# Performance work log

Measured on AMD Instinct MI355X. Metric: run time of the kernel, lower is better.

The kernel has to match this reference:

```python
import jax, jax.numpy as jnp
import numpy as np

EPS = 1e-6
R = 8


def _gram_schmidt(U, eps=EPS):
    # Modified Gram-Schmidt over the r columns of U (dim, r), matching the
    # sequential projection loop in HouseholderReflection.get_orthogonal_matrix.
    cols = []
    u0 = U[:, 0]
    cols.append(u0 / (jnp.linalg.norm(u0) + eps))
    r = U.shape[1]
    for i in range(1, r):
        ui = U[:, i]
        for j in range(i):
            ui = ui - jnp.dot(cols[j], ui) * cols[j]
        cols.append(ui / (jnp.linalg.norm(ui) + eps))
    return cols  # list of r unit vectors (dim,)


def _orthogonal_matrix(hra_u, eps=EPS):
    # Q = prod_i (I - 2 u_i u_i^T), applied as rank-1 updates: Q <- Q - 2 (Q u) u^T
    dim = hra_u.shape[0]
    cols = _gram_schmidt(hra_u, eps)
    Q = jnp.eye(dim, dtype=hra_u.dtype)
    for u in cols:
        Q = Q - 2.0 * jnp.outer(Q @ u, u)
    return Q  # (dim, dim)


def setup_inputs() -> dict:
    key = jax.random.key(0)
    k1, k2, k3, k4, k5 = jax.random.split(key, 5)
    N, D_IN, D_HID, D_OUT = 4096, 2048, 8192, 2048
    x = jax.random.normal(k1, (N, D_IN), dtype=jnp.float32)
    hra_u = jax.random.normal(k2, (D_IN, R), dtype=jnp.float32)
    W_random = jax.random.normal(k3, (D_IN, D_HID), dtype=jnp.float32) / np.sqrt(D_IN)
    W_out = jax.random.normal(k4, (D_HID, D_OUT), dtype=jnp.float32) / np.sqrt(D_HID)
    bias = jax.random.normal(k5, (D_OUT,), dtype=jnp.float32)
    return {"x": x, "hra_u": hra_u, "W_random": W_random, "W_out": W_out, "bias": bias}


def reference(x, hra_u, W_random, W_out, bias):
    # y = gelu(x @ (Q @ W_random)) @ W_out + bias  (torch nn.GELU = exact erf gelu)
    Q = _orthogonal_matrix(hra_u)
    W_t = Q @ W_random                      # (D_IN, D_HID)
    h = jax.nn.gelu(x @ W_t, approximate=False)  # (N, D_HID)
    return h @ W_out + bias                 # (N, D_OUT)
```

## Files before the change

### kernel.cpp

```cpp
#include <hip/hip_runtime.h>
#include <hip/hip_bf16.h>

typedef __bf16 bf16;
typedef __bf16 bf16x4 __attribute__((ext_vector_type(4)));
typedef __bf16 bf16x8 __attribute__((ext_vector_type(8)));
typedef float  f32x4  __attribute__((ext_vector_type(4)));

#define GAS __attribute__((address_space(1)))
#define LAS __attribute__((address_space(3)))

#define NROWS 4096
#define DIN   2048
#define DHID  8192
#define DOUT  2048

__device__ __forceinline__ void gload16(const void* g, void* l) {
    __builtin_amdgcn_global_load_lds((GAS void*)g, (LAS void*)l, 16, 0, 0);
}
template <int N> __device__ __forceinline__ void vmw() {
    asm volatile("s_waitcnt vmcnt(%0)" :: "n"(N) : "memory");
}
__device__ __forceinline__ void bsync() {
    asm volatile("" ::: "memory");
    __builtin_amdgcn_s_barrier();
    asm volatile("" ::: "memory");
}

__global__ __launch_bounds__(64) void gs_kernel(const float* __restrict__ U,
                                                float* __restrict__ Vt) {
    __shared__ float Vs[8][DIN];
    const int l = threadIdx.x;
    float u[32];
    for (int r = 0; r < 8; ++r) {
        #pragma unroll
        for (int s = 0; s < 32; ++s) u[s] = U[(size_t)(l * 32 + s) * 8 + r];
        for (int j = 0; j < r; ++j) {
            float d = 0.f;
            #pragma unroll
            for (int s = 0; s < 32; ++s) d += Vs[j][l * 32 + s] * u[s];
            #pragma unroll
            for (int o = 32; o >= 1; o >>= 1) d += __shfl_xor(d, o);
            #pragma unroll
            for (int s = 0; s < 32; ++s) u[s] -= d * Vs[j][l * 32 + s];
        }
        float nr = 0.f;
        #pragma unroll
        for (int s = 0; s < 32; ++s) nr += u[s] * u[s];
        #pragma unroll
        for (int o = 32; o >= 1; o >>= 1) nr += __shfl_xor(nr, o);
        const float inv = 1.f / (sqrtf(nr) + 1e-6f);
        #pragma unroll
        for (int s = 0; s < 32; ++s) {
            float v = u[s] * inv;
            Vs[r][l * 32 + s] = v;
            Vt[r * DIN + l * 32 + s] = v;
        }
        __syncthreads();
    }
}

__global__ __launch_bounds__(256) void p_kernel(const float* __restrict__ W,
                                                const float* __restrict__ Vt,
                                                float* __restrict__ P) {
    const int t = threadIdx.x;
    const int c = blockIdx.x * 64 + (t & 63);
    const int part = t >> 6;
    float acc[8] = {};
    const int i0 = part * 512;
    #pragma unroll 4
    for (int i = i0; i < i0 + 512; ++i) {
        float w = W[(size_t)i * DHID + c];
        #pragma unroll
        for (int r = 0; r < 8; ++r) acc[r] = fmaf(Vt[r * DIN + i], w, acc[r]);
    }
    __shared__ float red[4][8][64];
    #pragma unroll
    for (int r = 0; r < 8; ++r) red[part][r][t & 63] = acc[r];
    __syncthreads();
    for (int idx = t; idx < 512; idx += 256) {
        int r = idx >> 6, cc = idx & 63;
        P[(size_t)r * DHID + blockIdx.x * 64 + cc] =
            red[0][r][cc] + red[1][r][cc] + red[2][r][cc] + red[3][r][cc];
    }
}

__global__ __launch_bounds__(256) void xv_kernel(const float* __restrict__ x,
                                                 const float* __restrict__ Vt,
                                                 float* __restrict__ xV,
                                                 bf16* __restrict__ xb) {
    const int row = blockIdx.x * 4 + (threadIdx.x >> 6);
    const int l = threadIdx.x & 63;
    const float* xr = x + (size_t)row * DIN;
    bf16* xbr = xb + (size_t)row * DIN;
    float acc[8] = {};
    #pragma unroll
    for (int s = 0; s < 8; ++s) {
        const int c0 = (s * 64 + l) * 4;
        float4 v = *(const float4*)&xr[c0];
        bf16x4 o = { (bf16)v.x, (bf16)v.y, (bf16)v.z, (bf16)v.w };
        *(bf16x4*)&xbr[c0] = o;
        #pragma unroll
        for (int r = 0; r < 8; ++r) {
            float4 vt = *(const float4*)&Vt[r * DIN + c0];
            acc[r] = fmaf(v.x, vt.x, fmaf(v.y, vt.y, fmaf(v.z, vt.z, fmaf(v.w, vt.w, acc[r]))));
        }
    }
    #pragma unroll
    for (int r = 0; r < 8; ++r) {
        float d = acc[r];
        #pragma unroll
        for (int o = 32; o >= 1; o >>= 1) d += __shfl_xor(d, o);
        if (l == 0) xV[(size_t)row * 8 + r] = d;
    }
}

__global__ __launch_bounds__(256) void tconv_kernel(const float* __restrict__ in,
                                                    bf16* __restrict__ out,
                                                    int R, int C) {
    __shared__ bf16 tile[64][66];
    const int t = threadIdx.x;
    const int n0 = blockIdx.x * 64, k0 = blockIdx.y * 64;
    const int rr = t >> 4, c4 = (t & 15) * 4;
    #pragma unroll
    for (int q = 0; q < 4; ++q) {
        int row = k0 + rr + q * 16;
        float4 v = *(const float4*)&in[(size_t)row * C + n0 + c4];
        tile[c4 + 0][rr + q * 16] = (bf16)v.x;
        tile[c4 + 1][rr + q * 16] = (bf16)v.y;
        tile[c4 + 2][rr + q * 16] = (bf16)v.z;
        tile[c4 + 3][rr + q * 16] = (bf16)v.w;
    }
    __syncthreads();
    const int n = t >> 2, kk = (t & 3) * 16;
    unsigned int w[8];
    #pragma unroll
    for (int i = 0; i < 8; ++i) w[i] = *(const unsigned int*)&tile[n][kk + i * 2];
    uint4 lo = { w[0], w[1], w[2], w[3] }, hi = { w[4], w[5], w[6], w[7] };
    uint4* dst = (uint4*)&out[(size_t)(n0 + n) * R + k0 + kk];
    dst[0] = lo;
    dst[1] = hi;
}

__global__ __launch_bounds__(256) void redk(float* __restrict__ out,
                                            const float* __restrict__ p1,
                                            const float* __restrict__ bias) {
    const size_t i = (size_t)blockIdx.x * 256 + threadIdx.x;
    float4 a = ((const float4*)out)[i];
    float4 b = ((const float4*)p1)[i];
    const int c4 = (int)(i & (DOUT / 4 - 1)) * 4;
    float4 bb = *(const float4*)&bias[c4];
    float4 r = { a.x + b.x + bb.x, a.y + b.y + bb.y,
                 a.z + b.z + bb.z, a.w + b.w + bb.w };
    ((float4*)out)[i] = r;
}

template <int BM, int BN, int WM, int WN, int CR, int CC, int EPI>
__global__ __launch_bounds__(512) void gemm8p(const bf16* __restrict__ A,
                                              const bf16* __restrict__ Bt,
                                              const int N, const int nk, const int lda,
                                              const float* __restrict__ e0,
                                              const float* __restrict__ e1,
                                              void* __restrict__ Cout) {
    constexpr int MF = BM / (WM * 16);
    constexpr int NF = BN / (WN * 16);
    constexpr int ABYTES = BM * 64;
    constexpr int BUFB = (BM + BN) * 64;
    constexpr int LA = BM / 128, LB = BN / 128, LPT = LA + LB;
    __shared__ __align__(128) char lds[4 * BUFB];

    const int t = threadIdx.x;
    const int wid = t >> 6, lane = t & 63;
    const int wr = wid / WN, wc = wid % WN;
    const int lrow = lane & 15;
    const int lk2 = (lane >> 4) * 16;

    int bid = blockIdx.x, sk = 0;
    if constexpr (EPI == 2) { sk = bid & 1; bid >>= 1; }
    const int chunks_c = (N / BN) / CC;
    const int xc = bid & 7;
    const int ii = bid >> 3;
    const int bm = (xc / chunks_c) * CR + ii / CC;
    const int bn = (xc % chunks_c) * CC + ii % CC;

    const size_t koff = (size_t)sk * nk * 32;
    const bf16* Abase = A + (size_t)bm * BM * lda + koff;
    const bf16* Bbase = Bt + (size_t)bn * BN * lda + koff;

    const int ar0 = wr * (MF * 16) + lrow;
    const unsigned aoff = (unsigned)(ar0 * 64 + lk2) ^ (unsigned)(((ar0 >> 1) & 3) << 4);
    const int br0 = wc * (NF * 16) + lrow;
    const unsigned boff = (unsigned)ABYTES +
        ((unsigned)(br0 * 64 + lk2) ^ (unsigned)(((br0 >> 1) & 3) << 4));

    f32x4 acc[MF][NF] = {};

    auto STAGE = [&](int kt, int part) {
        const size_t ko = (size_t)kt * 32;
        char* dstb = lds + (kt & 3) * BUFB;
        if (part == 0) {
            #pragma unroll
            for (int i2 = 0; i2 < LA; ++i2) {
                const int lin = i2 * 512 + t;
                const int row = lin >> 2;
                const int c16 = (lin & 3) ^ ((lin >> 3) & 3);
                gload16(Abase + (size_t)row * lda + ko + c16 * 8,
                        dstb + (i2 * 512 + (t & 448)) * 16);
            }
        } else {
            #pragma unroll
            for (int i2 = 0; i2 < LB; ++i2) {
                const int lin = i2 * 512 + t;
                const int row = lin >> 2;
                const int c16 = (lin & 3) ^ ((lin >> 3) & 3);
                gload16(Bbase + (size_t)row * lda + ko + c16 * 8,
                        dstb + ABYTES + (i2 * 512 + (t & 448)) * 16);
            }
        }
    };

    auto TILE = [&](int kt, bool dostage) {
        const char* bp = lds + (kt & 3) * BUFB;
        bf16x8 av0[MF / 2], av1[MF / 2], bv[NF];
        #pragma unroll
        for (int m = 0; m < MF / 2; ++m)
            av0[m] = *(const bf16x8*)(bp + aoff + m * 1024);
        #pragma unroll
        for (int n = 0; n < NF; ++n)
            bv[n] = *(const bf16x8*)(bp + boff + n * 1024);
        if (dostage) STAGE(kt + 3, 0);
        __builtin_amdgcn_sched_barrier(0);
        bsync();
        __builtin_amdgcn_s_setprio(1);
        #pragma unroll
        for (int m = 0; m < MF / 2; ++m)
            #pragma unroll
            for (int n = 0; n < NF; ++n)
                acc[m][n] = __builtin_amdgcn_mfma_f32_16x16x32_bf16(av0[m], bv[n], acc[m][n], 0, 0, 0);
        __builtin_amdgcn_s_setprio(0);
        bsync();
        #pragma unroll
        for (int m = 0; m < MF / 2; ++m)
            av1[m] = *(const bf16x8*)(bp + aoff + (m + MF / 2) * 1024);
        if (dostage) STAGE(kt + 3, 1);
        __builtin_amdgcn_sched_barrier(0);
        bsync();
        __builtin_amdgcn_s_setprio(1);
        #pragma unroll
        for (int m = 0; m < MF / 2; ++m)
            #pragma unroll
            for (int n = 0; n < NF; ++n)
                acc[m + MF / 2][n] = __builtin_amdgcn_mfma_f32_16x16x32_bf16(av1[m], bv[n], acc[m + MF / 2][n], 0, 0, 0);
        __builtin_amdgcn_s_setprio(0);
    };

    #pragma unroll
    for (int p = 0; p < 3; ++p) { STAGE(p, 0); STAGE(p, 1); }
    vmw<2 * LPT>(); bsync();
    int kt = 0;
    for (; kt < nk - 3; ++kt) {
        TILE(kt, true);
        vmw<2 * LPT>();
        bsync();
    }
    TILE(kt, false); vmw<LPT>(); bsync(); ++kt;
    TILE(kt, false); vmw<0>();   bsync(); ++kt;
    TILE(kt, false); bsync();

    const int jrow = (lane >> 4) << 2;
    if constexpr (EPI == 1) {
        float* xVl = (float*)lds;
        float* Pl  = (float*)(lds + BM * 32);
        for (int idx = t; idx < BM * 8; idx += 512)
            xVl[idx] = e0[((size_t)bm * BM + (idx >> 3)) * 8 + (idx & 7)];
        for (int idx = t; idx < BN * 8; idx += 512)
            Pl[idx] = e1[(size_t)(idx / BN) * N + (size_t)bn * BN + (idx % BN)];
        bsync();
        bf16* outp = (bf16*)Cout;
        #pragma unroll
        for (int m = 0; m < MF; ++m)
            #pragma unroll
            for (int n = 0; n < NF; ++n)
                #pragma unroll
                for (int j = 0; j < 4; ++j) {
                    const int rl = wr * (MF * 16) + m * 16 + jrow + j;
                    const int cl = wc * (NF * 16) + n * 16 + lrow;
                    float v = acc[m][n][j];
                    float corr = 0.f;
                    #pragma unroll
                    for (int r = 0; r < 8; ++r)
                        corr = fmaf(xVl[rl * 8 + r], Pl[r * BN + cl], corr);
                    v = fmaf(-2.f, corr, v);
                    v = 0.5f * v * (1.f + erff(v * 0.70710678118654752440f));
                    outp[((size_t)bm * BM + rl) * N + bn * BN + cl] = (bf16)v;
                }
    } else {
        float* outp = sk ? const_cast<float*>(e1) : (float*)Cout;
        #pragma unroll
        for (int m = 0; m < MF; ++m)
            #pragma unroll
            for (int n = 0; n < NF; ++n)
                #pragma unroll
                for (int j = 0; j < 4; ++j) {
                    const int rl = wr * (MF * 16) + m * 16 + jrow + j;
                    const int cl = wc * (NF * 16) + n * 16 + lrow;
                    outp[((size_t)bm * BM + rl) * N + bn * BN + cl] = acc[m][n][j];
                }
    }
}

extern "C" void kernel_launch(void* const* d_in, const int* in_sizes, int n_in,
                              void* d_out, int out_size, void* d_ws, size_t ws_size,
                              hipStream_t stream) {
    const float* x     = (const float*)d_in[0];
    const float* hra_u = (const float*)d_in[1];
    const float* Wr    = (const float*)d_in[2];
    const float* Wo    = (const float*)d_in[3];
    const float* bias  = (const float*)d_in[4];
    float* out = (float*)d_out;
    char* ws = (char*)d_ws;

    float* Vt  = (float*)(ws + 0);
    float* P   = (float*)(ws + 65536);
    float* xV  = (float*)(ws + 327680);
    bf16*  xb  = (bf16*)(ws + 458752);
    bf16*  WrT = (bf16*)(ws + 17235968);
    bf16*  WoT = (bf16*)(ws + 50790400);
    bf16*  hb  = (bf16*)(ws + 84344832);
    float* p1  = (float*)(ws + 458752);

    gs_kernel<<<dim3(1), dim3(64), 0, stream>>>(hra_u, Vt);
    p_kernel<<<dim3(DHID / 64), dim3(256), 0, stream>>>(Wr, Vt, P);
    xv_kernel<<<dim3(NROWS / 4), dim3(256), 0, stream>>>(x, Vt, xV, xb);
    tconv_kernel<<<dim3(DHID / 64, DIN / 64), dim3(256), 0, stream>>>(Wr, WrT, DIN, DHID);
    tconv_kernel<<<dim3(DOUT / 64, DHID / 64), dim3(256), 0, stream>>>(Wo, WoT, DHID, DOUT);

    gemm8p<256, 256, 2, 4, 8, 8, 1><<<dim3(512), dim3(512), 0, stream>>>(
        xb, WrT, DHID, DIN / 32, DIN, xV, P, (void*)hb);
    gemm8p<256, 256, 2, 4, 4, 4, 2><<<dim3(256), dim3(512), 0, stream>>>(
        hb, WoT, DOUT, DHID / 64, DHID, nullptr, p1, (void*)out);
    redk<<<dim3((NROWS * DOUT) / 1024), dim3(256), 0, stream>>>(out, p1, bias);
}
```

Measured before the change: 640.2 us.

## Restructure GEMM pipeline to double-buffered 64-wide K tiles with four phases

The bf16 MFMA GEMM moves from a 4-deep ring of 32-wide K tiles to a 2-deep double buffer of 64-wide K tiles. Each tile is split into four quarter-stage phases, so a global-to-LDS load is interleaved with each MFMA block, with fewer barriers per unit of K. Barriers now wait on lgkmcnt, and scheduling fences are added. The p_kernel is also re-split into 32-column blocks with 8 K-parts for more parallelism. The trade-off is a shallower prefetch, which makes it harder to hide memory latency.

```diff
diff --git a/kernel.cpp b/kernel.cpp
--- a/kernel.cpp
+++ b/kernel.cpp
@@ -18,13 +18,9 @@
     __builtin_amdgcn_global_load_lds((GAS void*)g, (LAS void*)l, 16, 0, 0);
 }
 template <int N> __device__ __forceinline__ void vmw() {
-    asm volatile("s_waitcnt vmcnt(%0)" :: "n"(N) : "memory");
-}
-__device__ __forceinline__ void bsync() {
-    asm volatile("" ::: "memory");
-    __builtin_amdgcn_s_barrier();
-    asm volatile("" ::: "memory");
-}
+    asm volatile("s_waitcnt vmcnt(%0)" :: "n"(N));
+}
+__device__ __forceinline__ void SB() { __builtin_amdgcn_sched_barrier(0); }
 
 __global__ __launch_bounds__(64) void gs_kernel(const float* __restrict__ U,
                                                 float* __restrict__ Vt) {
@@ -63,24 +59,26 @@
                                                 const float* __restrict__ Vt,
                                                 float* __restrict__ P) {
     const int t = threadIdx.x;
-    const int c = blockIdx.x * 64 + (t & 63);
-    const int part = t >> 6;
+    const int c = blockIdx.x * 32 + (t & 31);
+    const int part = t >> 5;
     float acc[8] = {};
-    const int i0 = part * 512;
+    const int i0 = part * 256;
     #pragma unroll 4
-    for (int i = i0; i < i0 + 512; ++i) {
+    for (int i = i0; i < i0 + 256; ++i) {
         float w = W[(size_t)i * DHID + c];
         #pragma unroll
         for (int r = 0; r < 8; ++r) acc[r] = fmaf(Vt[r * DIN + i], w, acc[r]);
     }
-    __shared__ float red[4][8][64];
-    #pragma unroll
-    for (int r = 0; r < 8; ++r) red[part][r][t & 63] = acc[r];
+    __shared__ float red[8][8][32];
+    #pragma unroll
+    for (int r = 0; r < 8; ++r) red[part][r][t & 31] = acc[r];
     __syncthreads();
-    for (int idx = t; idx < 512; idx += 256) {
-        int r = idx >> 6, cc = idx & 63;
-        P[(size_t)r * DHID + blockIdx.x * 64 + cc] =
-            red[0][r][cc] + red[1][r][cc] + red[2][r][cc] + red[3][r][cc];
+    {
+        int r = t >> 5, cc = t & 31;
+        float s = 0.f;
+        #pragma unroll
+        for (int p = 0; p < 8; ++p) s += red[p][r][cc];
+        P[(size_t)r * DHID + blockIdx.x * 32 + cc] = s;
     }
 }
 
@@ -154,156 +152,165 @@
     ((float4*)out)[i] = r;
 }
 
-template <int BM, int BN, int WM, int WN, int CR, int CC, int EPI>
-__global__ __launch_bounds__(512) void gemm8p(const bf16* __restrict__ A,
+template <int CR, int CC, int EPI>
+__global__ __launch_bounds__(512) void gemm4p(const bf16* __restrict__ A,
                                               const bf16* __restrict__ Bt,
                                               const int N, const int nk, const int lda,
                                               const float* __restrict__ e0,
                                               const float* __restrict__ e1,
                                               void* __restrict__ Cout) {
-    constexpr int MF = BM / (WM * 16);
-    constexpr int NF = BN / (WN * 16);
-    constexpr int ABYTES = BM * 64;
-    constexpr int BUFB = (BM + BN) * 64;
-    constexpr int LA = BM / 128, LB = BN / 128, LPT = LA + LB;
-    __shared__ __align__(128) char lds[4 * BUFB];
-
+    __shared__ __align__(128) char lds[131072];
     const int t = threadIdx.x;
     const int wid = t >> 6, lane = t & 63;
-    const int wr = wid / WN, wc = wid % WN;
+    const int wr = wid >> 2, wc = wid & 3;
     const int lrow = lane & 15;
     const int lk2 = (lane >> 4) * 16;
 
     int bid = blockIdx.x, sk = 0;
     if constexpr (EPI == 2) { sk = bid & 1; bid >>= 1; }
-    const int chunks_c = (N / BN) / CC;
+    const int chunks_c = (N >> 8) / CC;
     const int xc = bid & 7;
     const int ii = bid >> 3;
     const int bm = (xc / chunks_c) * CR + ii / CC;
     const int bn = (xc % chunks_c) * CC + ii % CC;
 
-    const size_t koff = (size_t)sk * nk * 32;
-    const bf16* Abase = A + (size_t)bm * BM * lda + koff;
-    const bf16* Bbase = Bt + (size_t)bn * BN * lda + koff;
-
-    const int ar0 = wr * (MF * 16) + lrow;
-    const unsigned aoff = (unsigned)(ar0 * 64 + lk2) ^ (unsigned)(((ar0 >> 1) & 3) << 4);
-    const int br0 = wc * (NF * 16) + lrow;
-    const unsigned boff = (unsigned)ABYTES +
-        ((unsigned)(br0 * 64 + lk2) ^ (unsigned)(((br0 >> 1) & 3) << 4));
-
-    f32x4 acc[MF][NF] = {};
-
-    auto STAGE = [&](int kt, int part) {
-        const size_t ko = (size_t)kt * 32;
-        char* dstb = lds + (kt & 3) * BUFB;
-        if (part == 0) {
-            #pragma unroll
-            for (int i2 = 0; i2 < LA; ++i2) {
-                const int lin = i2 * 512 + t;
-                const int row = lin >> 2;
-                const int c16 = (lin & 3) ^ ((lin >> 3) & 3);
-                gload16(Abase + (size_t)row * lda + ko + c16 * 8,
-                        dstb + (i2 * 512 + (t & 448)) * 16);
-            }
-        } else {
-            #pragma unroll
-            for (int i2 = 0; i2 < LB; ++i2) {
-                const int lin = i2 * 512 + t;
-                const int row = lin >> 2;
-                const int c16 = (lin & 3) ^ ((lin >> 3) & 3);
-                gload16(Bbase + (size_t)row * lda + ko + c16 * 8,
-                        dstb + ABYTES + (i2 * 512 + (t & 448)) * 16);
-            }
+    const size_t koff = (size_t)sk * nk * 64;
+    const bf16* Abase = A + (size_t)bm * 256 * lda + koff;
+    const bf16* Bbase = Bt + (size_t)bn * 256 * lda + koff;
+
+    const unsigned aswz = (unsigned)(((lrow >> 1) & 3) << 4);
+    const unsigned aoff0 = (unsigned)((wr * 128 + lrow) * 64 + lk2) ^ aswz;
+    const unsigned boff0 = (unsigned)((wc * 64 + lrow) * 64 + lk2) ^ aswz;
+
+    f32x4 acc[8][4] = {};
+
+    auto STAGEQ = [&](int kt, int q) {
+        const bf16* Pb = (q < 2) ? Abase : Bbase;
+        const size_t kq = (size_t)kt * 64 + (size_t)(q & 1) * 32;
+        char* reg = lds + (kt & 1) * 65536 + q * 16384;
+        #pragma unroll
+        for (int i2 = 0; i2 < 2; ++i2) {
+            const int lin = i2 * 512 + t;
+            const int row = lin >> 2;
+            const int g = (lin & 3) ^ ((lin >> 3) & 3);
+            gload16(Pb + (size_t)row * lda + kq + g * 8,
+                    reg + (i2 * 512 + (t & 448)) * 16);
         }
     };
 
-    auto TILE = [&](int kt, bool dostage) {
-        const char* bp = lds + (kt & 3) * BUFB;
-        bf16x8 av0[MF / 2], av1[MF / 2], bv[NF];
-        #pragma unroll
-        for (int m = 0; m < MF / 2; ++m)
-            av0[m] = *(const bf16x8*)(bp + aoff + m * 1024);
-        #pragma unroll
-        for (int n = 0; n < NF; ++n)
-            bv[n] = *(const bf16x8*)(bp + boff + n * 1024);
-        if (dostage) STAGE(kt + 3, 0);
-        __builtin_amdgcn_sched_barrier(0);
-        bsync();
+    auto PH_SYNC = [&]() {
+        SB();
+        __builtin_amdgcn_s_barrier();
+        asm volatile("s_waitcnt lgkmcnt(0)");
+        SB();
+    };
+
+    auto TILE64 = [&](int kt, bool dostage) {
+        const char* bp = lds + (kt & 1) * 65536;
+        bf16x8 av[4], bv[4], aw[4], av2[4], bv2[4], aw2[4];
+        #pragma unroll
+        for (int m = 0; m < 4; ++m) av[m] = *(const bf16x8*)(bp + aoff0 + m * 1024);
+        #pragma unroll
+        for (int n = 0; n < 4; ++n) bv[n] = *(const bf16x8*)(bp + 32768 + boff0 + n * 1024);
+        if (dostage) STAGEQ(kt + 1, 0);
+        PH_SYNC();
         __builtin_amdgcn_s_setprio(1);
         #pragma unroll
-        for (int m = 0; m < MF / 2; ++m)
-            #pragma unroll
-            for (int n = 0; n < NF; ++n)
-                acc[m][n] = __builtin_amdgcn_mfma_f32_16x16x32_bf16(av0[m], bv[n], acc[m][n], 0, 0, 0);
+        for (int m = 0; m < 4; ++m)
+            #pragma unroll
+            for (int n = 0; n < 4; ++n)
+                acc[m][n] = __builtin_amdgcn_mfma_f32_16x16x32_bf16(av[m], bv[n], acc[m][n], 0, 0, 0);
         __builtin_amdgcn_s_setprio(0);
-        bsync();
-        #pragma unroll
-        for (int m = 0; m < MF / 2; ++m)
-            av1[m] = *(const bf16x8*)(bp + aoff + (m + MF / 2) * 1024);
-        if (dostage) STAGE(kt + 3, 1);
-        __builtin_amdgcn_sched_barrier(0);
-        bsync();
+        #pragma unroll
+        for (int m = 0; m < 4; ++m) aw[m] = *(const bf16x8*)(bp + aoff0 + (m + 4) * 1024);
+        if (dostage) { STAGEQ(kt + 1, 2); SB(); vmw<4>(); }
+        else         { SB(); vmw<0>(); }
+        PH_SYNC();
         __builtin_amdgcn_s_setprio(1);
         #pragma unroll
-        for (int m = 0; m < MF / 2; ++m)
-            #pragma unroll
-            for (int n = 0; n < NF; ++n)
-                acc[m + MF / 2][n] = __builtin_amdgcn_mfma_f32_16x16x32_bf16(av1[m], bv[n], acc[m + MF / 2][n], 0, 0, 0);
+        for (int m = 0; m < 4; ++m)
+            #pragma unroll
+            for (int n = 0; n < 4; ++n)
+                acc[m + 4][n] = __builtin_amdgcn_mfma_f32_16x16x32_bf16(aw[m], bv[n], acc[m + 4][n], 0, 0, 0);
+        __builtin_amdgcn_s_setprio(0);
+        #pragma unroll
+        for (int m = 0; m < 4; ++m) av2[m] = *(const bf16x8*)(bp + 16384 + aoff0 + m * 1024);
+        #pragma unroll
+        for (int n = 0; n < 4; ++n) bv2[n] = *(const bf16x8*)(bp + 49152 + boff0 + n * 1024);
+        if (dostage) STAGEQ(kt + 1, 1);
+        PH_SYNC();
+        __builtin_amdgcn_s_setprio(1);
+        #pragma unroll
+        for (int m = 0; m < 4; ++m)
+            #pragma unroll
+            for (int n = 0; n < 4; ++n)
+                acc[m][n] = __builtin_amdgcn_mfma_f32_16x16x32_bf16(av2[m], bv2[n], acc[m][n], 0, 0, 0);
+        __builtin_amdgcn_s_setprio(0);
+        #pragma unroll
+        for (int m = 0; m < 4; ++m) aw2[m] = *(const bf16x8*)(bp + 16384 + aoff0 + (m + 4) * 1024);
+        if (dostage) { STAGEQ(kt + 1, 3); SB(); vmw<4>(); }
+        PH_SYNC();
+        __builtin_amdgcn_s_setprio(1);
+        #pragma unroll
+        for (int m = 0; m < 4; ++m)
+            #pragma unroll
+            for (int n = 0; n < 4; ++n)
+                acc[m + 4][n] = __builtin_amdgcn_mfma_f32_16x16x32_bf16(aw2[m], bv2[n], acc[m + 4][n], 0, 0, 0);
         __builtin_amdgcn_s_setprio(0);
     };
 
-    #pragma unroll
-    for (int p = 0; p < 3; ++p) { STAGE(p, 0); STAGE(p, 1); }
-    vmw<2 * LPT>(); bsync();
-    int kt = 0;
-    for (; kt < nk - 3; ++kt) {
-        TILE(kt, true);
-        vmw<2 * LPT>();
-        bsync();
-    }
-    TILE(kt, false); vmw<LPT>(); bsync(); ++kt;
-    TILE(kt, false); vmw<0>();   bsync(); ++kt;
-    TILE(kt, false); bsync();
+    STAGEQ(0, 0); STAGEQ(0, 2); STAGEQ(0, 1); STAGEQ(0, 3);
+    SB(); vmw<4>();
+    __builtin_amdgcn_s_barrier();
+    SB();
+
+    for (int kt = 0; kt < nk - 1; ++kt) TILE64(kt, true);
+    TILE64(nk - 1, false);
 
     const int jrow = (lane >> 4) << 2;
     if constexpr (EPI == 1) {
+        SB();
+        __builtin_amdgcn_s_barrier();
+        SB();
         float* xVl = (float*)lds;
-        float* Pl  = (float*)(lds + BM * 32);
-        for (int idx = t; idx < BM * 8; idx += 512)
-            xVl[idx] = e0[((size_t)bm * BM + (idx >> 3)) * 8 + (idx & 7)];
-        for (int idx = t; idx < BN * 8; idx += 512)
-            Pl[idx] = e1[(size_t)(idx / BN) * N + (size_t)bn * BN + (idx % BN)];
-        bsync();
+        float* Pl  = (float*)(lds + 8192);
+        for (int idx = t; idx < 2048; idx += 512)
+            xVl[idx] = e0[((size_t)bm * 256 + (idx >> 3)) * 8 + (idx & 7)];
+        for (int idx = t; idx < 2048; idx += 512)
+            Pl[idx] = e1[(size_t)(idx >> 8) * N + (size_t)bn * 256 + (idx & 255)];
+        asm volatile("s_waitcnt lgkmcnt(0)");
+        SB();
+        __builtin_amdgcn_s_barrier();
+        SB();
         bf16* outp = (bf16*)Cout;
         #pragma unroll
-        for (int m = 0; m < MF; ++m)
-            #pragma unroll
-            for (int n = 0; n < NF; ++n)
+        for (int m = 0; m < 8; ++m)
+            #pragma unroll
+            for (int n = 0; n < 4; ++n)
                 #pragma unroll
                 for (int j = 0; j < 4; ++j) {
-                    const int rl = wr * (MF * 16) + m * 16 + jrow + j;
-                    const int cl = wc * (NF * 16) + n * 16 + lrow;
+                    const int rl = wr * 128 + m * 16 + jrow + j;
+                    const int cl = wc * 64 + n * 16 + lrow;
                     float v = acc[m][n][j];
                     float corr = 0.f;
                     #pragma unroll
                     for (int r = 0; r < 8; ++r)
-                        corr = fmaf(xVl[rl * 8 + r], Pl[r * BN + cl], corr);
+                        corr = fmaf(xVl[rl * 8 + r], Pl[r * 256 + cl], corr);
                     v = fmaf(-2.f, corr, v);
                     v = 0.5f * v * (1.f + erff(v * 0.70710678118654752440f));
-                    outp[((size_t)bm * BM + rl) * N + bn * BN + cl] = (bf16)v;
+                    outp[((size_t)bm * 256 + rl) * N + bn * 256 + cl] = (bf16)v;
                 }
     } else {
         float* outp = sk ? const_cast<float*>(e1) : (float*)Cout;
         #pragma unroll
-        for (int m = 0; m < MF; ++m)
-            #pragma unroll
-            for (int n = 0; n < NF; ++n)
+        for (int m = 0; m < 8; ++m)
+            #pragma unroll
+            for (int n = 0; n < 4; ++n)
                 #pragma unroll
                 for (int j = 0; j < 4; ++j) {
-                    const int rl = wr * (MF * 16) + m * 16 + jrow + j;
-                    const int cl = wc * (NF * 16) + n * 16 + lrow;
-                    outp[((size_t)bm * BM + rl) * N + bn * BN + cl] = acc[m][n][j];
+                    const int rl = wr * 128 + m * 16 + jrow + j;
+                    const int cl = wc * 64 + n * 16 + lrow;
+                    outp[((size_t)bm * 256 + rl) * N + bn * 256 + cl] = acc[m][n][j];
                 }
     }
 }
@@ -329,14 +336,14 @@
     float* p1  = (float*)(ws + 458752);
 
     gs_kernel<<<dim3(1), dim3(64), 0, stream>>>(hra_u, Vt);
-    p_kernel<<<dim3(DHID / 64), dim3(256), 0, stream>>>(Wr, Vt, P);
+    p_kernel<<<dim3(DHID / 32), dim3(256), 0, stream>>>(Wr, Vt, P);
     xv_kernel<<<dim3(NROWS / 4), dim3(256), 0, stream>>>(x, Vt, xV, xb);
     tconv_kernel<<<dim3(DHID / 64, DIN / 64), dim3(256), 0, stream>>>(Wr, WrT, DIN, DHID);
     tconv_kernel<<<dim3(DOUT / 64, DHID / 64), dim3(256), 0, stream>>>(Wo, WoT, DHID, DOUT);
 
-    gemm8p<256, 256, 2, 4, 8, 8, 1><<<dim3(512), dim3(512), 0, stream>>>(
-        xb, WrT, DHID, DIN / 32, DIN, xV, P, (void*)hb);
-    gemm8p<256, 256, 2, 4, 4, 4, 2><<<dim3(256), dim3(512), 0, stream>>>(
-        hb, WoT, DOUT, DHID / 64, DHID, nullptr, p1, (void*)out);
+    gemm4p<8, 8, 1><<<dim3(512), dim3(512), 0, stream>>>(
+        xb, WrT, DHID, DIN / 64, DIN, xV, P, (void*)hb);
+    gemm4p<4, 4, 2><<<dim3(256), dim3(512), 0, stream>>>(
+        hb, WoT, DOUT, DHID / 128, DHID, nullptr, p1, (void*)out);
     redk<<<dim3((NROWS * DOUT) / 1024), dim3(256), 0, stream>>>(out, p1, bias);
 }
```

Result: faster. 573.1 us (-10.5%).
